# Performance work log

Measured on AMD Instinct MI355X. Metric: run time of the kernel, lower is better.

## Reference

```python
import jax, jax.numpy as jnp
import numpy as np

B, N, C, K = 8, 4096, 256, 8192

def setup_inputs() -> dict:
    key = jax.random.key(0)
    k1, k2 = jax.random.split(key)
    z_e_x = jax.random.normal(k1, (B, N, C), dtype=jnp.float32)
    # codebook initialized like the torch module: normal(0,1) rescaled so mean row norm = sqrt(D)
    cb = jax.random.normal(k2, (K, C), dtype=jnp.float32)
    cur = jnp.mean(jnp.linalg.norm(cb, axis=1))
    cb = cb * (jnp.sqrt(jnp.float32(C)) / cur)
    return {"z_e_x": z_e_x, "codebook": cb}

def reference(z_e_x, codebook):
    """VQ straight-through forward: returns (codes, idx, distances).
    codes: [B,N,C] nearest codebook vectors; idx: [B,N] int32 indices;
    distances: [B,N] min squared L2 distances."""
    b, n, c = z_e_x.shape
    x = z_e_x.astype(jnp.float32).reshape(b * n, c)          # [BN, C]
    cb = codebook.astype(jnp.float32)                        # [K, C]
    cb_sq = jnp.sum(cb * cb, axis=1)                         # [K]
    x_sq = jnp.sum(x * x, axis=1, keepdims=True)             # [BN,1]
    l2 = x_sq + cb_sq[None, :] - 2.0 * (x @ cb.T)            # [BN, K]
    idx_flat = jnp.argmin(l2, axis=1)                        # [BN]
    min_vals = jnp.min(l2, axis=1)                           # [BN]
    codes = jnp.take(cb, idx_flat, axis=0).reshape(b, n, c).astype(z_e_x.dtype)
    idx = idx_flat.reshape(b, n)
    distances = min_vals.reshape(b, n).astype(z_e_x.dtype)
    return codes, idx, distances
```

## Files before the change

### kernel.cpp

```cpp
#include <hip/hip_runtime.h>
#include <hip/hip_bf16.h>
#include <stdint.h>


#define M_ROWS 32768
#define KCODES 8192
#define CDIM   256
#define BM 128
#define BNT 256
#define BK 32
#define NTILES 32
#define NREC 32
#define MARGIN 0.75f

typedef _Float16 f16x8 __attribute__((ext_vector_type(8)));
typedef _Float16 f16x4 __attribute__((ext_vector_type(4)));
typedef float    f32x4 __attribute__((ext_vector_type(4)));

#define WAITV(N) asm volatile("s_waitcnt vmcnt(" #N ")" ::: "memory")

__device__ __forceinline__ unsigned umin2(unsigned a, unsigned b) { return a < b ? a : b; }
__device__ __forceinline__ unsigned umax2(unsigned a, unsigned b) { return a > b ? a : b; }

__global__ void vq_prep(const float* __restrict__ x, const float* __restrict__ cb,
                        _Float16* __restrict__ xhi, _Float16* __restrict__ cbhi,
                        float* __restrict__ xsq, float* __restrict__ cbsq) {
  const int wave = threadIdx.x >> 6, lane = threadIdx.x & 63;
  const int row = blockIdx.x * 4 + wave;
  const float* src;
  _Float16* dhi;
  float* dsq;
  if (row < M_ROWS) {
    src = x + (size_t)row * CDIM;  dhi = xhi + (size_t)row * CDIM;  dsq = xsq + row;
  } else {
    const int r = row - M_ROWS;
    src = cb + (size_t)r * CDIM;   dhi = cbhi + (size_t)r * CDIM;   dsq = cbsq + r;
  }
  const float4 v = *(const float4*)(src + lane * 4);
  f16x4 h;
  h[0] = (_Float16)(v.x * 64.0f); h[1] = (_Float16)(v.y * 64.0f);
  h[2] = (_Float16)(v.z * 64.0f); h[3] = (_Float16)(v.w * 64.0f);
  *(f16x4*)(dhi + lane * 4) = h;
  float s = v.x * v.x + v.y * v.y + v.z * v.z + v.w * v.w;
  #pragma unroll
  for (int off = 32; off > 0; off >>= 1) s += __shfl_down(s, off, 64);
  if (lane == 0) *dsq = s;
}

__device__ __forceinline__ void gl16p(const void* g, void* l) {
  __builtin_amdgcn_global_load_lds(
      (const __attribute__((address_space(1))) unsigned int*)g,
      (__attribute__((address_space(3))) unsigned int*)l, 16, 0, 0);
}

__global__ __launch_bounds__(512, 2) void vq_pass1(
    const _Float16* __restrict__ xhi, const _Float16* __restrict__ cbhi,
    const float* __restrict__ cbsqg, uint2* __restrict__ srec) {
  extern __shared__ char smem[];
  _Float16* sA  = (_Float16*)smem;
  _Float16* sB  = (_Float16*)(smem + 65536);
  float*    sCq = (float*)(smem + 65536 + 65536);

  const int tid  = threadIdx.x;
  const int wave = tid >> 6, lane = tid & 63;
  const int quad = lane >> 4, l15 = lane & 15;
  const int mbase = blockIdx.x * BM;
  const int wrow = (wave >> 2) * 64;
  const int wcol = (wave & 3) * 64;

  {
    const int ar = lane >> 5;
    const int as = lane & 31;
    #pragma unroll
    for (int t = 0; t < 8; ++t) {
      const int rb  = (wave * 8 + t) * 2;
      const int row = rb + ar;
      const int slot = as ^ (row & 7);
      gl16p(xhi + (size_t)(mbase + row) * CDIM + slot * 8, sA + rb * CDIM);
    }
  }

  const int srl  = lane >> 2;
  const int scol = (((lane & 3) ^ ((lane >> 3) & 3)) << 3);
  const int fcol = ((quad ^ ((l15 >> 1) & 3)) << 3);
  const int asw  = l15 & 7;

  auto stageB = [&](int nts, int kss, int bufidx) {
    const int cb0 = nts * BNT, kofs = kss * BK;
    _Float16* dst = sB + bufidx * (BNT * BK);
    #pragma unroll
    for (int t = 0; t < 2; ++t) {
      const int rb = wave * 32 + t * 16;
      gl16p(cbhi + (size_t)(cb0 + rb + srl) * CDIM + kofs + scol, dst + rb * BK);
    }
  };
  auto stageCq = [&](int nts) {
    gl16p(cbsqg + nts * BNT + lane * 4, sCq + (nts & 1) * BNT);
  };

  stageB(0, 0, 0); stageCq(0);
  stageB(0, 1, 1);

  unsigned k1[4][4], k2[4][4];

  for (int nt = 0; nt < NTILES; ++nt) {
    const bool lastnt = (nt == NTILES - 1);
    if ((nt & 3) == 0) {
      #pragma unroll
      for (int mf = 0; mf < 4; ++mf)
        #pragma unroll
        for (int i = 0; i < 4; ++i) { k1[mf][i] = 0x7fffffffu; k2[mf][i] = 0x7fffffffu; }
    }

    f32x4 acc[4][4];
    #pragma unroll
    for (int mf = 0; mf < 4; ++mf)
      #pragma unroll
      for (int nf = 0; nf < 4; ++nf) {
        f32x4 z = {0.0f, 0.0f, 0.0f, 0.0f};
        acc[mf][nf] = z;
      }

    #pragma unroll
    for (int ks = 0; ks < 8; ++ks) {
      if (ks <= 5) {
        stageB(nt, ks + 2, (ks + 2) & 3);
      } else if (ks == 6) {
        if (!lastnt) { stageB(nt + 1, 0, 0); stageCq(nt + 1); }
      } else {
        if (!lastnt) stageB(nt + 1, 1, 1);
      }
      if (ks <= 5)      WAITV(4);
      else if (ks == 6) { if (!lastnt) WAITV(5); else WAITV(2); }
      else              { if (!lastnt) WAITV(5); else WAITV(0); }
      __builtin_amdgcn_s_barrier();
      asm volatile("" ::: "memory");

      const _Float16* sBc = sB + (ks & 3) * (BNT * BK);
      f16x8 ah[4];
      #pragma unroll
      for (int mf = 0; mf < 4; ++mf) {
        const int arow = wrow + mf * 16 + l15;
        const int aslot = (ks * 4 + quad) ^ asw;
        ah[mf] = *(const f16x8*)(sA + arow * CDIM + aslot * 8);
      }
      __builtin_amdgcn_s_setprio(1);
      #pragma unroll
      for (int nf = 0; nf < 4; ++nf) {
        const f16x8 bh = *(const f16x8*)(sBc + (wcol + nf * 16 + l15) * BK + fcol);
        #pragma unroll
        for (int mf = 0; mf < 4; ++mf)
          acc[mf][nf] = __builtin_amdgcn_mfma_f32_16x16x32_f16(ah[mf], bh, acc[mf][nf], 0, 0, 0);
      }
      __builtin_amdgcn_s_setprio(0);
    }

    #pragma unroll
    for (int nf = 0; nf < 4; ++nf) {
      const int cwl = wcol + nf * 16 + l15;
      const int col = nt * BNT + cwl;
      const float cq16 = fmaf(sCq[(nt & 1) * BNT + cwl], 16.0f, 32768.0f);
      #pragma unroll
      for (int mf = 0; mf < 4; ++mf)
        #pragma unroll
        for (int i = 0; i < 4; ++i) {
          const float kf = fmaf(acc[mf][nf][i], -0.0078125f, cq16);
          const unsigned key = ((unsigned)kf << 13) | (unsigned)col;
          k2[mf][i] = umin2(k2[mf][i], umax2(k1[mf][i], key));
          k1[mf][i] = umin2(k1[mf][i], key);
        }
    }

    if ((nt & 3) == 3) {
      const int g = (nt >> 2) * 4 + (wave & 3);
      #pragma unroll
      for (int mf = 0; mf < 4; ++mf)
        #pragma unroll
        for (int i = 0; i < 4; ++i) {
          unsigned a1 = k1[mf][i], a2 = k2[mf][i];
          #pragma unroll
          for (int m = 1; m <= 8; m <<= 1) {
            const unsigned o1 = (unsigned)__shfl_xor((int)a1, m, 64);
            const unsigned o2 = (unsigned)__shfl_xor((int)a2, m, 64);
            a2 = umin2(umin2(a2, o2), umax2(a1, o1));
            a1 = umin2(a1, o1);
          }
          if (l15 == 0) {
            const int rl = wrow + mf * 16 + quad * 4 + i;
            uint2 r; r.x = a1; r.y = a2;
            srec[(size_t)(mbase + rl) * NREC + g] = r;
          }
        }
    }
  }
}

__global__ void vq_finalize(const float* __restrict__ x, const float* __restrict__ cb,
                            const float* __restrict__ xsq, const float* __restrict__ cbsq,
                            const uint2* __restrict__ srec,
                            float* __restrict__ outIdx, float* __restrict__ outDist,
                            float* __restrict__ codes) {
  const int wave = threadIdx.x >> 6, lane = threadIdx.x & 63;
  const int row = blockIdx.x * 4 + wave;
  uint2 rec;
  if (lane < NREC) rec = srec[(size_t)row * NREC + lane];
  else { rec.x = 0x7fffffffu; rec.y = 0x7fffffffu; }
  const float v1 = (float)(rec.x >> 13) * 0.0625f - 2048.0f;
  const float v2 = (float)(rec.y >> 13) * 0.0625f - 2048.0f;
  const int c1 = (int)(rec.x & 8191u);
  const int c2 = (int)(rec.y & 8191u);

  float gm = v1;
  #pragma unroll
  for (int m = 1; m <= 32; m <<= 1) gm = fminf(gm, __shfl_xor(gm, m, 64));
  const float thr = gm + MARGIN;
  unsigned long long mask1 = __ballot(v1 <= thr);
  unsigned long long mask2 = __ballot(v2 <= thr);

  const float4 xv = *(const float4*)(x + (size_t)row * CDIM + lane * 4);
  const float xq = xsq[row];
  float best = __builtin_inff(); int bidx = 1 << 30;

  #pragma unroll
  for (int pass = 0; pass < 2; ++pass) {
    unsigned long long m = pass ? mask2 : mask1;
    const int fi = pass ? c2 : c1;
    while (m) {
      const int g = __builtin_ctzll((long long)m); m &= m - 1;
      const int ci = __shfl(fi, g, 64);
      const float4 cv = *(const float4*)(cb + (size_t)ci * CDIM + lane * 4);
      float s = xv.x * cv.x + xv.y * cv.y + xv.z * cv.z + xv.w * cv.w;
      #pragma unroll
      for (int mm = 1; mm <= 32; mm <<= 1) s += __shfl_xor(s, mm, 64);
      const float dist = xq + cbsq[ci] - 2.0f * s;
      if (dist < best || (dist == best && ci < bidx)) { best = dist; bidx = ci; }
    }
  }

  if (lane == 0) { outIdx[row] = (float)bidx; outDist[row] = best; }
  const float4 cw = *(const float4*)(cb + (size_t)bidx * CDIM + lane * 4);
  *(float4*)(codes + (size_t)row * CDIM + lane * 4) = cw;
}

extern "C" void kernel_launch(void* const* d_in, const int* in_sizes, int n_in,
                              void* d_out, int out_size, void* d_ws, size_t ws_size,
                              hipStream_t stream) {
  const float* x  = (const float*)d_in[0];
  const float* cb = (const float*)d_in[1];
  float* out = (float*)d_out;

  char* w = (char*)d_ws;
  _Float16* xhi  = (_Float16*)(w);
  _Float16* cbhi = (_Float16*)(w + 16777216);
  float*    xsq  = (float*)   (w + 20971520);
  float*    cbsq = (float*)   (w + 21102592);
  uint2*    srec = (uint2*)   (w + 21135360);

  vq_prep<<<(M_ROWS + KCODES) / 4, 256, 0, stream>>>(x, cb, xhi, cbhi, xsq, cbsq);
  const size_t smem = 65536 + 65536 + 2048;
  vq_pass1<<<dim3(M_ROWS / BM), 512, smem, stream>>>(xhi, cbhi, cbsq, srec);
  vq_finalize<<<M_ROWS / 4, 256, 0, stream>>>(x, cb, xsq, cbsq, srec,
                                              out + 8388608, out + 8421376, out);
}
```

Baseline: 283.4 us.

## Give each wave a private codebook LDS slice to drop block barriers

Each wave now stages only the 64 codebook columns it consumes into its own double-buffered LDS region. This removes the per-k-step block-wide barrier and relies on per-wave vmcnt waits instead. The codebook squared norms are loaded straight into registers and prefetched one tile ahead, replacing the shared LDS staging. In exchange, prefetch depth drops from four buffers to two with a full vmcnt(0) wait every step, so load latency is less hidden. The launch-bounds occupancy hint is also removed.

Measured after the change: 279.4 us. Within noise of the previous version (-1.4%).

```diff
diff --git a/kernel.cpp b/kernel.cpp
--- a/kernel.cpp
+++ b/kernel.cpp
@@ -53,20 +53,20 @@
       (__attribute__((address_space(3))) unsigned int*)l, 16, 0, 0);
 }
 
-__global__ __launch_bounds__(512, 2) void vq_pass1(
+__global__ __launch_bounds__(512) void vq_pass1(
     const _Float16* __restrict__ xhi, const _Float16* __restrict__ cbhi,
     const float* __restrict__ cbsqg, uint2* __restrict__ srec) {
   extern __shared__ char smem[];
-  _Float16* sA  = (_Float16*)smem;
-  _Float16* sB  = (_Float16*)(smem + 65536);
-  float*    sCq = (float*)(smem + 65536 + 65536);
+  _Float16* sA = (_Float16*)smem;
+  _Float16* sB = (_Float16*)(smem + 65536);
 
   const int tid  = threadIdx.x;
   const int wave = tid >> 6, lane = tid & 63;
   const int quad = lane >> 4, l15 = lane & 15;
   const int mbase = blockIdx.x * BM;
   const int wrow = (wave >> 2) * 64;
-  const int wcol = (wave & 3) * 64;
+  const int q    = wave & 3;
+  const int wcol = q * 64;
 
   {
     const int ar = lane >> 5;
@@ -85,21 +85,25 @@
   const int fcol = ((quad ^ ((l15 >> 1) & 3)) << 3);
   const int asw  = l15 & 7;
 
-  auto stageB = [&](int nts, int kss, int bufidx) {
-    const int cb0 = nts * BNT, kofs = kss * BK;
-    _Float16* dst = sB + bufidx * (BNT * BK);
-    #pragma unroll
-    for (int t = 0; t < 2; ++t) {
-      const int rb = wave * 32 + t * 16;
-      gl16p(cbhi + (size_t)(cb0 + rb + srl) * CDIM + kofs + scol, dst + rb * BK);
-    }
+  _Float16* sBw = sB + wave * 4096;
+
+  auto stageB = [&](int nts, int kss, int buf) {
+    const int c0 = nts * BNT + wcol;
+    const int kofs = kss * BK;
+    _Float16* dst = sBw + buf * 2048;
+    #pragma unroll
+    for (int t = 0; t < 4; ++t)
+      gl16p(cbhi + (size_t)(c0 + t * 16 + srl) * CDIM + kofs + scol, dst + t * 512);
   };
-  auto stageCq = [&](int nts) {
-    gl16p(cbsqg + nts * BNT + lane * 4, sCq + (nts & 1) * BNT);
-  };
-
-  stageB(0, 0, 0); stageCq(0);
-  stageB(0, 1, 1);
+
+  float cq_cur[4], cq_nxt[4];
+  #pragma unroll
+  for (int j = 0; j < 4; ++j) cq_cur[j] = cbsqg[wcol + j * 16 + l15];
+
+  stageB(0, 0, 0);
+  WAITV(4);
+  __builtin_amdgcn_s_barrier();
+  asm volatile("" ::: "memory");
 
   unsigned k1[4][4], k2[4][4];
 
@@ -123,31 +127,26 @@
 
     #pragma unroll
     for (int ks = 0; ks < 8; ++ks) {
-      if (ks <= 5) {
-        stageB(nt, ks + 2, (ks + 2) & 3);
-      } else if (ks == 6) {
-        if (!lastnt) { stageB(nt + 1, 0, 0); stageCq(nt + 1); }
-      } else {
-        if (!lastnt) stageB(nt + 1, 1, 1);
+      WAITV(0);
+      asm volatile("" ::: "memory");
+      if (ks < 7)        stageB(nt, ks + 1, (ks + 1) & 1);
+      else if (!lastnt)  stageB(nt + 1, 0, 0);
+      if (ks == 6 && !lastnt) {
+        #pragma unroll
+        for (int j = 0; j < 4; ++j)
+          cq_nxt[j] = cbsqg[(nt + 1) * BNT + wcol + j * 16 + l15];
       }
-      if (ks <= 5)      WAITV(4);
-      else if (ks == 6) { if (!lastnt) WAITV(5); else WAITV(2); }
-      else              { if (!lastnt) WAITV(5); else WAITV(0); }
-      __builtin_amdgcn_s_barrier();
-      asm volatile("" ::: "memory");
-
-      const _Float16* sBc = sB + (ks & 3) * (BNT * BK);
+
+      const _Float16* sBc = sBw + (ks & 1) * 2048;
+      const int aslot = (ks * 4 + quad) ^ asw;
       f16x8 ah[4];
       #pragma unroll
-      for (int mf = 0; mf < 4; ++mf) {
-        const int arow = wrow + mf * 16 + l15;
-        const int aslot = (ks * 4 + quad) ^ asw;
-        ah[mf] = *(const f16x8*)(sA + arow * CDIM + aslot * 8);
-      }
+      for (int mf = 0; mf < 4; ++mf)
+        ah[mf] = *(const f16x8*)(sA + (wrow + mf * 16 + l15) * CDIM + aslot * 8);
       __builtin_amdgcn_s_setprio(1);
       #pragma unroll
       for (int nf = 0; nf < 4; ++nf) {
-        const f16x8 bh = *(const f16x8*)(sBc + (wcol + nf * 16 + l15) * BK + fcol);
+        const f16x8 bh = *(const f16x8*)(sBc + (nf * 16 + l15) * BK + fcol);
         #pragma unroll
         for (int mf = 0; mf < 4; ++mf)
           acc[mf][nf] = __builtin_amdgcn_mfma_f32_16x16x32_f16(ah[mf], bh, acc[mf][nf], 0, 0, 0);
@@ -157,9 +156,8 @@
 
     #pragma unroll
     for (int nf = 0; nf < 4; ++nf) {
-      const int cwl = wcol + nf * 16 + l15;
-      const int col = nt * BNT + cwl;
-      const float cq16 = fmaf(sCq[(nt & 1) * BNT + cwl], 16.0f, 32768.0f);
+      const int col = nt * BNT + wcol + nf * 16 + l15;
+      const float cq16 = fmaf(cq_cur[nf], 16.0f, 32768.0f);
       #pragma unroll
       for (int mf = 0; mf < 4; ++mf)
         #pragma unroll
@@ -172,7 +170,7 @@
     }
 
     if ((nt & 3) == 3) {
-      const int g = (nt >> 2) * 4 + (wave & 3);
+      const int g = (nt >> 2) * 4 + q;
       #pragma unroll
       for (int mf = 0; mf < 4; ++mf)
         #pragma unroll
@@ -192,6 +190,9 @@
           }
         }
     }
+
+    #pragma unroll
+    for (int j = 0; j < 4; ++j) cq_cur[j] = cq_nxt[j];
   }
 }
 
@@ -257,7 +258,7 @@
   uint2*    srec = (uint2*)   (w + 21135360);
 
   vq_prep<<<(M_ROWS + KCODES) / 4, 256, 0, stream>>>(x, cb, xhi, cbhi, xsq, cbsq);
-  const size_t smem = 65536 + 65536 + 2048;
+  const size_t smem = 65536 + 65536;
   vq_pass1<<<dim3(M_ROWS / BM), 512, smem, stream>>>(xhi, cbhi, cbsq, srec);
   vq_finalize<<<M_ROWS / 4, 256, 0, stream>>>(x, cb, xsq, cbsq, srec,
                                               out + 8388608, out + 8421376, out);
```
